# Optimization experiments

Measured on AMD Instinct MI355X. Metric: run time of the kernel, lower is better.

## Reference

```python
import jax, jax.numpy as jnp
import numpy as np


def setup_inputs() -> dict:
    key = jax.random.key(0)
    ks = jax.random.split(key, 8)
    B, L, D, N, K = 4, 4096, 1024, 64, 4
    return {
        "x": jax.random.normal(ks[0], (B, L, D), dtype=jnp.float32),
        "conv_w": jax.random.normal(ks[1], (K, 1, D), dtype=jnp.float32) * 0.1,
        "conv_b": jnp.zeros((D,), dtype=jnp.float32),
        "Wp": jax.random.normal(ks[2], (D, 2 * N), dtype=jnp.float32) * (1.0 / np.sqrt(D)),
        "bp": jnp.zeros((2 * N,), dtype=jnp.float32),
        "Ws": jax.random.normal(ks[3], (D, N), dtype=jnp.float32) * (1.0 / np.sqrt(D)),
        "bs": jnp.zeros((N,), dtype=jnp.float32),
        "A_log": jax.random.normal(ks[4], (N,), dtype=jnp.float32) * 0.02,
        "dt_log": jax.random.normal(ks[5], (N,), dtype=jnp.float32) * 0.02,
        "Wo": jax.random.normal(ks[6], (N, D), dtype=jnp.float32) * (1.0 / np.sqrt(N)),
        "bo": jnp.zeros((D,), dtype=jnp.float32),
    }


def reference(x, conv_w, conv_b, Wp, bp, Ws, bs, A_log, dt_log, Wo, bo):
    B, L, D = x.shape
    K = conv_w.shape[0]
    N = Ws.shape[1]

    # causal depthwise conv: left-pad by K-1, sum K shifted slices (K is tiny)
    x_pad = jnp.pad(x, ((0, 0), (K - 1, 0), (0, 0)))
    conv = conv_b + sum(x_pad[:, k:k + L, :] * conv_w[k, 0] for k in range(K))

    proj = conv @ Wp + bp                     # [B, L, 2N]
    B_t = jax.nn.softplus(proj[..., :N])      # [B, L, N]
    C_t = jnp.tanh(proj[..., N:])             # [B, L, N]
    u = x @ Ws + bs                           # [B, L, N]

    A = -jax.nn.softplus(A_log)               # [N]
    dt = jax.nn.softplus(dt_log)              # [N]
    decay = 1.0 + dt * A                      # [N]

    def step(state, inputs):
        u_t, b_t, c_t = inputs                # each [B, N]
        state = decay * state + dt * b_t * u_t
        return state, c_t * state

    init = jnp.zeros((B, N), dtype=x.dtype)
    xs = tuple(jnp.swapaxes(a, 0, 1) for a in (u, B_t, C_t))  # time-major
    _, ys = jax.lax.scan(step, init, xs, unroll=4)            # [L, B, N]
    y = jnp.swapaxes(ys, 0, 1)                                # [B, L, N]
    return y @ Wo + bo                                        # [B, L, D]
```

## Files before the change

### kernel.cpp

```cpp
#include <hip/hip_runtime.h>

#define B_ 4
#define L_ 4096
#define D_ 1024
#define N_ 64

typedef _Float16 f16;
typedef __attribute__((ext_vector_type(8))) _Float16 half8;
typedef __attribute__((ext_vector_type(4))) float f32x4;

__device__ __forceinline__ float softplus_f(float x) {
    return fmaxf(x, 0.0f) + log1pf(__expf(-fabsf(x)));
}

__device__ __forceinline__ float tanh_f(float x) {
    float xc = fminf(fmaxf(x, -15.0f), 15.0f);
    float e = __expf(2.0f * xc);
    return (e - 1.0f) / (e + 1.0f);
}

__global__ __launch_bounds__(256) void k_prepw(
    const float* __restrict__ Wp, const float* __restrict__ Ws,
    const float* __restrict__ Wo, f16* __restrict__ WT, f16* __restrict__ WoT)
{
    int gid = blockIdx.x * 256 + threadIdx.x;
    if (gid < 24576) {
        int r = gid >> 7, kg = gid & 127;
        const float* src; int ncol, c;
        if (r < 128) { src = Wp; ncol = 128; c = r; }
        else         { src = Ws; ncol = 64;  c = r - 128; }
        f16 h[8];
        #pragma unroll
        for (int j = 0; j < 8; j++)
            h[j] = (f16)src[(size_t)(kg * 8 + j) * ncol + c];
        *(uint4*)&WT[(size_t)r * 1024 + kg * 8] = *(uint4*)h;
    } else {
        int g2 = gid - 24576;
        int d = g2 >> 3, ng = g2 & 7;
        f16 h[8];
        #pragma unroll
        for (int j = 0; j < 8; j++)
            h[j] = (f16)Wo[(size_t)(ng * 8 + j) * D_ + d];
        *(uint4*)&WoT[(size_t)d * 64 + ng * 8] = *(uint4*)h;
    }
}

__global__ __launch_bounds__(256) void k_frontend(
    const float* __restrict__ x, const float* __restrict__ conv_w,
    const float* __restrict__ conv_b, const f16* __restrict__ WT,
    const float* __restrict__ bp, const float* __restrict__ bs,
    const float* __restrict__ dt_log,
    f16* __restrict__ zT, f16* __restrict__ cT)
{
    __shared__ __align__(16) char smem[25664];
    f16*   xh  = (f16*)smem;
    f16*   ch  = (f16*)(smem + 2880);
    float* cwS = (float*)(smem + 5184);
    float* sE  = (float*)smem;

    const int tid = threadIdx.x;
    const int w = tid >> 6, lane = tid & 63;
    const int r = lane & 15, q = lane >> 4;
    const int T0 = blockIdx.x * 16;
    const int bb = T0 >> 12;
    const int l0 = T0 & (L_ - 1);
    const int cw0 = w * 48;

    f32x4 acc[3] = {};
    float4 rA, rB;

    #pragma unroll
    for (int i = 0; i < 5; i++) {
        int idx = tid + 256 * i;
        float4 v = (idx < 1024) ? ((const float4*)conv_w)[idx]
                                : ((const float4*)conv_b)[idx - 1024];
        ((float4*)cwS)[idx] = v;
    }

    #define LDX(c0)                                                          \
        {                                                                    \
            {                                                                \
                int row = tid >> 4, g = tid & 15;                            \
                int l = l0 + row - 4;                                        \
                float4 v = make_float4(0.f, 0.f, 0.f, 0.f);                  \
                if (l >= 0)                                                  \
                    v = *(const float4*)&x[((size_t)(bb * L_ + l)) * D_      \
                                           + (c0) + g * 4];                  \
                rA = v;                                                      \
            }                                                                \
            if (tid < 64) {                                                  \
                int row = 16 + (tid >> 4), g = tid & 15;                     \
                int l = l0 + row - 4;               \
                rB = *(const float4*)&x[((size_t)(bb * L_ + l)) * D_         \
                                        + (c0) + g * 4];                     \
            }                                                                \
        }

    LDX(0);
    for (int c = 0; c < 16; c++) {
        __syncthreads();
        {
            int row = tid >> 4, g = tid & 15;
            f16 h[4] = {(f16)rA.x, (f16)rA.y, (f16)rA.z, (f16)rA.w};
            *(uint2*)&xh[row * 72 + g * 4] = *(uint2*)h;
            if (tid < 64) {
                int row2 = 16 + (tid >> 4);
                f16 h2[4] = {(f16)rB.x, (f16)rB.y, (f16)rB.z, (f16)rB.w};
                *(uint2*)&xh[row2 * 72 + g * 4] = *(uint2*)h2;
            }
        }
        __syncthreads();
        if (c < 15) LDX((c + 1) * 64);

        const int k0 = c * 64;

        half8 af[2][3];
        #pragma unroll
        for (int ks = 0; ks < 2; ks++)
            #pragma unroll
            for (int mf = 0; mf < 3; mf++)
                af[ks][mf] = *(const half8*)&WT[
                    (size_t)(cw0 + mf * 16 + r) * 1024 + k0 + ks * 32 + q * 8];

        {
            const int row = tid >> 4;
            const int d4 = (tid & 15) * 4;
            const int dg = k0 + d4;
            f32x4 w0 = *(const f32x4*)&cwS[dg];
            f32x4 w1 = *(const f32x4*)&cwS[1024 + dg];
            f32x4 w2 = *(const f32x4*)&cwS[2048 + dg];
            f32x4 w3 = *(const f32x4*)&cwS[3072 + dg];
            f32x4 cb = *(const f32x4*)&cwS[4096 + dg];
            f16 x0[4], x1[4], x2[4], x3[4], ho[4];
            *(uint2*)x0 = *(const uint2*)&xh[(row + 1) * 72 + d4];
            *(uint2*)x1 = *(const uint2*)&xh[(row + 2) * 72 + d4];
            *(uint2*)x2 = *(const uint2*)&xh[(row + 3) * 72 + d4];
            *(uint2*)x3 = *(const uint2*)&xh[(row + 4) * 72 + d4];
            #pragma unroll
            for (int j = 0; j < 4; j++) {
                float s = cb[j];
                s = fmaf(w0[j], (float)x0[j], s);
                s = fmaf(w1[j], (float)x1[j], s);
                s = fmaf(w2[j], (float)x2[j], s);
                s = fmaf(w3[j], (float)x3[j], s);
                ho[j] = (f16)s;
            }
            *(uint2*)&ch[row * 72 + d4] = *(uint2*)ho;
        }
        __syncthreads();

        const bool needC = (cw0 < 128);
        const bool needR = (cw0 + 32 >= 128);
        #pragma unroll
        for (int ks = 0; ks < 2; ks++) {
            const int kl = ks * 32 + q * 8;
            half8 bc = {}, br = {};
            if (needC) bc = *(const half8*)&ch[r * 72 + kl];
            if (needR) br = *(const half8*)&xh[(r + 4) * 72 + kl];
            #pragma unroll
            for (int mf = 0; mf < 3; mf++) {
                const bool useConv = (cw0 + mf * 16) < 128;
                acc[mf] = __builtin_amdgcn_mfma_f32_16x16x32_f16(
                    af[ks][mf], useConv ? bc : br, acc[mf], 0, 0, 0);
            }
        }
    }

    float* sB = sE;
    float* sC = sE + 16 * 68;
    float* sU = sE + 2 * 16 * 68;
    __syncthreads();
    #pragma unroll
    for (int mf = 0; mf < 3; mf++) {
        const int cb4 = cw0 + mf * 16 + q * 4;
        const int seg = cb4 >> 6;
        const int cl = cb4 & 63;
        const float4 bb4 = (seg == 2) ? *(const float4*)&bs[cl]
                                      : *(const float4*)&bp[cb4];
        float* dst = (seg == 0) ? sB : (seg == 1 ? sC : sU);
        const int t = r;
        float v0 = acc[mf][0] + bb4.x;
        float v1 = acc[mf][1] + bb4.y;
        float v2 = acc[mf][2] + bb4.z;
        float v3 = acc[mf][3] + bb4.w;
        if (seg == 0) {
            v0 = softplus_f(v0); v1 = softplus_f(v1);
            v2 = softplus_f(v2); v3 = softplus_f(v3);
        } else if (seg == 1) {
            v0 = tanh_f(v0); v1 = tanh_f(v1);
            v2 = tanh_f(v2); v3 = tanh_f(v3);
        }
        float4 vv = {v0, v1, v2, v3};
        *(float4*)&dst[t * 68 + cl] = vv;
    }
    __syncthreads();

    {
        const int n = tid >> 2, tg = tid & 3;
        const float dtv = softplus_f(dt_log[n]);
        f16 hz[4], hc[4];
        #pragma unroll
        for (int j = 0; j < 4; j++) {
            const int t = tg * 4 + j;
            hz[j] = (f16)(dtv * sB[t * 68 + n] * sU[t * 68 + n]);
            hc[j] = (f16)sC[t * 68 + n];
        }
        size_t o = ((size_t)(bb * N_ + n)) * L_ + l0 + tg * 4;
        *(uint2*)&zT[o] = *(uint2*)hz;
        *(uint2*)&cT[o] = *(uint2*)hc;
    }
    #undef LDX
}

__global__ __launch_bounds__(64) void k_scan(
    const f16* __restrict__ zT, const f16* __restrict__ cT,
    const float* __restrict__ A_log, const float* __restrict__ dt_log,
    f16* __restrict__ yH)
{
    __shared__ float zs[L_];
    __shared__ float cs[L_];
    const int bn = blockIdx.x;
    const int n = bn & (N_ - 1);
    const int lane = threadIdx.x;
    const f16* zp = zT + (size_t)bn * L_;
    const f16* cp = cT + (size_t)bn * L_;

    for (int it = 0; it < 8; it++) {
        int i = lane * 8 + it * 512;
        uint4 rz = *(const uint4*)(zp + i);
        uint4 rc = *(const uint4*)(cp + i);
        const f16* hz = (const f16*)&rz;
        const f16* hc = (const f16*)&rc;
        #pragma unroll
        for (int k = 0; k < 8; k++) {
            zs[i + k] = (float)hz[k];
            cs[i + k] = (float)hc[k];
        }
    }
    __syncthreads();

    float dtv = softplus_f(dt_log[n]);
    float Av = -softplus_f(A_log[n]);
    float dec = fmaf(dtv, Av, 1.0f);

    float s = 0.0f;
    const int base = lane * 64;
    #pragma unroll
    for (int j = 0; j < 64; j++) s = fmaf(dec, s, zs[base + j]);

    float d2 = dec * dec, d4 = d2 * d2, d8 = d4 * d4;
    float d16 = d8 * d8, d32 = d16 * d16, d64 = d32 * d32;

    float Ag = d64, Bg = s;
    #pragma unroll
    for (int off = 1; off < 64; off <<= 1) {
        float Ap = __shfl_up(Ag, off);
        float Bp = __shfl_up(Bg, off);
        if (lane >= off) { Bg = fmaf(Ag, Bp, Bg); Ag *= Ap; }
    }
    float carry = __shfl_up(Bg, 1);
    if (lane == 0) carry = 0.0f;

    float st = carry;
    #pragma unroll
    for (int j = 0; j < 64; j++) {
        st = fmaf(dec, st, zs[base + j]);
        zs[base + j] = cs[base + j] * st;
    }
    __syncthreads();
    f16* yp = yH + (size_t)bn * L_;
    for (int i = lane * 8; i < L_; i += 512) {
        f16 h[8];
        #pragma unroll
        for (int k = 0; k < 8; k++) h[k] = (f16)zs[i + k];
        *(uint4*)&yp[i] = *(uint4*)h;
    }
}

__global__ __launch_bounds__(256) void k_out(
    const f16* __restrict__ yH, const f16* __restrict__ WoT,
    const float* __restrict__ bo, float* __restrict__ out)
{
    __shared__ __align__(16) f16 ys[64 * 72];
    const int tid = threadIdx.x;
    const int w = tid >> 6, lane = tid & 63;
    const int r = lane & 15, q = lane >> 4;
    const int T0 = blockIdx.x * 64;
    const int bb = T0 >> 12, l0 = T0 & (L_ - 1);
    const int dw = blockIdx.y * 128 + w * 32;

    {
        const int n = tid & 63, tg = tid >> 6;
        #pragma unroll
        for (int h2 = 0; h2 < 2; h2++) {
            uint4 v = *(const uint4*)&yH[((size_t)(bb * N_ + n)) * L_ + l0 + tg * 16 + h2 * 8];
            const f16* hh = (const f16*)&v;
            #pragma unroll
            for (int j = 0; j < 8; j++)
                ys[(tg * 16 + h2 * 8 + j) * 72 + n] = hh[j];
        }
    }
    __syncthreads();

    f32x4 acc[2][4] = {};
    #pragma unroll
    for (int ks = 0; ks < 2; ks++) {
        const int kk = ks * 32 + q * 8;
        half8 af[2];
        #pragma unroll
        for (int mf = 0; mf < 2; mf++)
            af[mf] = *(const half8*)&WoT[(size_t)(dw + mf * 16 + r) * 64 + kk];
        #pragma unroll
        for (int nf = 0; nf < 4; nf++) {
            half8 bf = *(const half8*)&ys[(nf * 16 + r) * 72 + kk];
            #pragma unroll
            for (int mf = 0; mf < 2; mf++)
                acc[mf][nf] = __builtin_amdgcn_mfma_f32_16x16x32_f16(
                    af[mf], bf, acc[mf][nf], 0, 0, 0);
        }
    }

    #pragma unroll
    for (int mf = 0; mf < 2; mf++) {
        const int d = dw + mf * 16 + q * 4;
        const float4 bb4 = *(const float4*)&bo[d];
        #pragma unroll
        for (int nf = 0; nf < 4; nf++) {
            const int t = T0 + nf * 16 + r;
            float4 o = {acc[mf][nf][0] + bb4.x, acc[mf][nf][1] + bb4.y,
                        acc[mf][nf][2] + bb4.z, acc[mf][nf][3] + bb4.w};
            *(float4*)&out[(size_t)t * D_ + d] = o;
        }
    }
}

extern "C" void kernel_launch(void* const* d_in, const int* in_sizes, int n_in,
                              void* d_out, int out_size, void* d_ws, size_t ws_size,
                              hipStream_t stream) {
    const float* x      = (const float*)d_in[0];
    const float* conv_w = (const float*)d_in[1];
    const float* conv_b = (const float*)d_in[2];
    const float* Wp     = (const float*)d_in[3];
    const float* bp     = (const float*)d_in[4];
    const float* Ws     = (const float*)d_in[5];
    const float* bs     = (const float*)d_in[6];
    const float* A_log  = (const float*)d_in[7];
    const float* dt_log = (const float*)d_in[8];
    const float* Wo     = (const float*)d_in[9];
    const float* bo     = (const float*)d_in[10];
    float* out = (float*)d_out;

    char* wsp = (char*)d_ws;
    f16* WT  = (f16*)wsp;
    f16* WoT = (f16*)(wsp + 393216);
    f16* zT  = (f16*)(wsp + 524288);
    f16* cT  = (f16*)(wsp + 2621440);
    f16* yH  = (f16*)(wsp + 4718592);

    k_prepw<<<dim3(128), dim3(256), 0, stream>>>(Wp, Ws, Wo, WT, WoT);
    k_frontend<<<dim3(B_ * L_ / 16), dim3(256), 0, stream>>>(
        x, conv_w, conv_b, WT, bp, bs, dt_log, zT, cT);
    k_scan<<<dim3(B_ * N_), dim3(64), 0, stream>>>(zT, cT, A_log, dt_log, yH);
    k_out<<<dim3(B_ * L_ / 64, D_ / 128), dim3(256), 0, stream>>>(yH, WoT, bo, out);
}
```

Measured before the change: 198.1 us.

## Stage whole x tile in LDS for frontend and widen scan to four waves

The frontend now loads the full 20x1024 x tile into LDS at once (fp16, padded stride), computes the causal conv for all 16 rows in one pass using a sliding register window, and then runs a single uninterrupted MFMA loop over K. This drops the per-chunk double-buffered load/sync structure. LDS use grows to about 75KB per block, which cuts occupancy. The scan kernel moves from 64 to 256 threads with padded shared indexing and a two-level (wave, then cross-wave) scan, shortening each thread's serial chain from 64 to 16 steps.

```diff
diff --git a/kernel.cpp b/kernel.cpp
--- a/kernel.cpp
+++ b/kernel.cpp
@@ -45,6 +45,7 @@
     }
 }
 
+#define XS 1040
 __global__ __launch_bounds__(256) void k_frontend(
     const float* __restrict__ x, const float* __restrict__ conv_w,
     const float* __restrict__ conv_b, const f16* __restrict__ WT,
@@ -52,11 +53,10 @@
     const float* __restrict__ dt_log,
     f16* __restrict__ zT, f16* __restrict__ cT)
 {
-    __shared__ __align__(16) char smem[25664];
-    f16*   xh  = (f16*)smem;
-    f16*   ch  = (f16*)(smem + 2880);
-    float* cwS = (float*)(smem + 5184);
-    float* sE  = (float*)smem;
+    __shared__ __align__(16) char smem[74880];
+    f16*   xh = (f16*)smem;
+    f16*   ch = (f16*)(smem + 41600);
+    float* sE = (float*)smem;
 
     const int tid = threadIdx.x;
     const int w = tid >> 6, lane = tid & 63;
@@ -66,104 +66,75 @@
     const int l0 = T0 & (L_ - 1);
     const int cw0 = w * 48;
 
-    f32x4 acc[3] = {};
-    float4 rA, rB;
-
-    #pragma unroll
-    for (int i = 0; i < 5; i++) {
-        int idx = tid + 256 * i;
-        float4 v = (idx < 1024) ? ((const float4*)conv_w)[idx]
-                                : ((const float4*)conv_b)[idx - 1024];
-        ((float4*)cwS)[idx] = v;
-    }
-
-    #define LDX(c0)                                                          \
-        {                                                                    \
-            {                                                                \
-                int row = tid >> 4, g = tid & 15;                            \
-                int l = l0 + row - 4;                                        \
-                float4 v = make_float4(0.f, 0.f, 0.f, 0.f);                  \
-                if (l >= 0)                                                  \
-                    v = *(const float4*)&x[((size_t)(bb * L_ + l)) * D_      \
-                                           + (c0) + g * 4];                  \
-                rA = v;                                                      \
-            }                                                                \
-            if (tid < 64) {                                                  \
-                int row = 16 + (tid >> 4), g = tid & 15;                     \
-                int l = l0 + row - 4;               \
-                rB = *(const float4*)&x[((size_t)(bb * L_ + l)) * D_         \
-                                        + (c0) + g * 4];                     \
-            }                                                                \
-        }
-
-    LDX(0);
-    for (int c = 0; c < 16; c++) {
-        __syncthreads();
-        {
-            int row = tid >> 4, g = tid & 15;
-            f16 h[4] = {(f16)rA.x, (f16)rA.y, (f16)rA.z, (f16)rA.w};
-            *(uint2*)&xh[row * 72 + g * 4] = *(uint2*)h;
-            if (tid < 64) {
-                int row2 = 16 + (tid >> 4);
-                f16 h2[4] = {(f16)rB.x, (f16)rB.y, (f16)rB.z, (f16)rB.w};
-                *(uint2*)&xh[row2 * 72 + g * 4] = *(uint2*)h2;
-            }
-        }
-        __syncthreads();
-        if (c < 15) LDX((c + 1) * 64);
-
-        const int k0 = c * 64;
-
-        half8 af[2][3];
-        #pragma unroll
-        for (int ks = 0; ks < 2; ks++)
-            #pragma unroll
-            for (int mf = 0; mf < 3; mf++)
-                af[ks][mf] = *(const half8*)&WT[
-                    (size_t)(cw0 + mf * 16 + r) * 1024 + k0 + ks * 32 + q * 8];
-
-        {
-            const int row = tid >> 4;
-            const int d4 = (tid & 15) * 4;
-            const int dg = k0 + d4;
-            f32x4 w0 = *(const f32x4*)&cwS[dg];
-            f32x4 w1 = *(const f32x4*)&cwS[1024 + dg];
-            f32x4 w2 = *(const f32x4*)&cwS[2048 + dg];
-            f32x4 w3 = *(const f32x4*)&cwS[3072 + dg];
-            f32x4 cb = *(const f32x4*)&cwS[4096 + dg];
-            f16 x0[4], x1[4], x2[4], x3[4], ho[4];
-            *(uint2*)x0 = *(const uint2*)&xh[(row + 1) * 72 + d4];
-            *(uint2*)x1 = *(const uint2*)&xh[(row + 2) * 72 + d4];
-            *(uint2*)x2 = *(const uint2*)&xh[(row + 3) * 72 + d4];
-            *(uint2*)x3 = *(const uint2*)&xh[(row + 4) * 72 + d4];
+    #pragma unroll
+    for (int s = 0; s < 20; s++) {
+        int idx = tid + 256 * s;
+        int row = idx >> 8, g = idx & 255;
+        int l = l0 + row - 4;
+        float4 v = make_float4(0.f, 0.f, 0.f, 0.f);
+        if (l >= 0)
+            v = *(const float4*)&x[((size_t)(bb * L_ + l)) * D_ + g * 4];
+        f16 h[4] = {(f16)v.x, (f16)v.y, (f16)v.z, (f16)v.w};
+        *(uint2*)&xh[row * XS + g * 4] = *(uint2*)h;
+    }
+    __syncthreads();
+
+    {
+        const int d0 = tid * 4;
+        const float4 w0 = *(const float4*)&conv_w[0 * D_ + d0];
+        const float4 w1 = *(const float4*)&conv_w[1 * D_ + d0];
+        const float4 w2 = *(const float4*)&conv_w[2 * D_ + d0];
+        const float4 w3 = *(const float4*)&conv_w[3 * D_ + d0];
+        const float4 cb = *(const float4*)&conv_b[d0];
+        const float cwv[4][4] = {{w0.x,w0.y,w0.z,w0.w},{w1.x,w1.y,w1.z,w1.w},
+                                 {w2.x,w2.y,w2.z,w2.w},{w3.x,w3.y,w3.z,w3.w}};
+        const float cbv[4] = {cb.x, cb.y, cb.z, cb.w};
+        uint2 win[4];
+        win[0] = *(const uint2*)&xh[1 * XS + d0];
+        win[1] = *(const uint2*)&xh[2 * XS + d0];
+        win[2] = *(const uint2*)&xh[3 * XS + d0];
+        #pragma unroll
+        for (int t = 0; t < 16; t++) {
+            win[3] = *(const uint2*)&xh[(t + 4) * XS + d0];
+            const f16* x0 = (const f16*)&win[0];
+            const f16* x1 = (const f16*)&win[1];
+            const f16* x2 = (const f16*)&win[2];
+            const f16* x3 = (const f16*)&win[3];
+            f16 ho[4];
             #pragma unroll
             for (int j = 0; j < 4; j++) {
-                float s = cb[j];
-                s = fmaf(w0[j], (float)x0[j], s);
-                s = fmaf(w1[j], (float)x1[j], s);
-                s = fmaf(w2[j], (float)x2[j], s);
-                s = fmaf(w3[j], (float)x3[j], s);
+                float s = cbv[j];
+                s = fmaf(cwv[0][j], (float)x0[j], s);
+                s = fmaf(cwv[1][j], (float)x1[j], s);
+                s = fmaf(cwv[2][j], (float)x2[j], s);
+                s = fmaf(cwv[3][j], (float)x3[j], s);
                 ho[j] = (f16)s;
             }
-            *(uint2*)&ch[row * 72 + d4] = *(uint2*)ho;
-        }
-        __syncthreads();
-
-        const bool needC = (cw0 < 128);
-        const bool needR = (cw0 + 32 >= 128);
-        #pragma unroll
-        for (int ks = 0; ks < 2; ks++) {
-            const int kl = ks * 32 + q * 8;
-            half8 bc = {}, br = {};
-            if (needC) bc = *(const half8*)&ch[r * 72 + kl];
-            if (needR) br = *(const half8*)&xh[(r + 4) * 72 + kl];
-            #pragma unroll
-            for (int mf = 0; mf < 3; mf++) {
-                const bool useConv = (cw0 + mf * 16) < 128;
-                acc[mf] = __builtin_amdgcn_mfma_f32_16x16x32_f16(
-                    af[ks][mf], useConv ? bc : br, acc[mf], 0, 0, 0);
-            }
-        }
+            *(uint2*)&ch[t * XS + d0] = *(uint2*)ho;
+            win[0] = win[1]; win[1] = win[2]; win[2] = win[3];
+        }
+    }
+    __syncthreads();
+
+    f32x4 acc[3] = {};
+    const bool needC = (cw0 < 128);
+    const bool needR = (cw0 + 32 >= 128);
+    const bool uc0 = (cw0      < 128);
+    const bool uc1 = (cw0 + 16 < 128);
+    const bool uc2 = (cw0 + 32 < 128);
+    const int klq = q * 8;
+    #pragma unroll 4
+    for (int j = 0; j < 32; j++) {
+        const int kk = j * 32 + klq;
+        half8 a0 = *(const half8*)&WT[(size_t)(cw0 +      r) * 1024 + kk];
+        half8 a1 = *(const half8*)&WT[(size_t)(cw0 + 16 + r) * 1024 + kk];
+        half8 a2 = *(const half8*)&WT[(size_t)(cw0 + 32 + r) * 1024 + kk];
+        half8 bc = {}, br = {};
+        if (needC) bc = *(const half8*)&ch[r * XS + kk];
+        if (needR) br = *(const half8*)&xh[(r + 4) * XS + kk];
+        acc[0] = __builtin_amdgcn_mfma_f32_16x16x32_f16(a0, uc0 ? bc : br, acc[0], 0, 0, 0);
+        acc[1] = __builtin_amdgcn_mfma_f32_16x16x32_f16(a1, uc1 ? bc : br, acc[1], 0, 0, 0);
+        acc[2] = __builtin_amdgcn_mfma_f32_16x16x32_f16(a2, uc2 ? bc : br, acc[2], 0, 0, 0);
     }
 
     float* sB = sE;
@@ -178,7 +149,6 @@
         const float4 bb4 = (seg == 2) ? *(const float4*)&bs[cl]
                                       : *(const float4*)&bp[cb4];
         float* dst = (seg == 0) ? sB : (seg == 1 ? sC : sU);
-        const int t = r;
         float v0 = acc[mf][0] + bb4.x;
         float v1 = acc[mf][1] + bb4.y;
         float v2 = acc[mf][2] + bb4.z;
@@ -191,7 +161,7 @@
             v2 = tanh_f(v2); v3 = tanh_f(v3);
         }
         float4 vv = {v0, v1, v2, v3};
-        *(float4*)&dst[t * 68 + cl] = vv;
+        *(float4*)&dst[r * 68 + cl] = vv;
     }
     __syncthreads();
 
@@ -209,32 +179,36 @@
         *(uint2*)&zT[o] = *(uint2*)hz;
         *(uint2*)&cT[o] = *(uint2*)hc;
     }
-    #undef LDX
-}
-
-__global__ __launch_bounds__(64) void k_scan(
+}
+#undef XS
+
+#define ZI(i) ((i) + ((i) >> 4))
+__global__ __launch_bounds__(256) void k_scan(
     const f16* __restrict__ zT, const f16* __restrict__ cT,
     const float* __restrict__ A_log, const float* __restrict__ dt_log,
     f16* __restrict__ yH)
 {
-    __shared__ float zs[L_];
-    __shared__ float cs[L_];
+    __shared__ float zs[4352];
+    __shared__ float cs[4352];
+    __shared__ float sA[4], sB[4];
     const int bn = blockIdx.x;
     const int n = bn & (N_ - 1);
-    const int lane = threadIdx.x;
+    const int tid = threadIdx.x;
+    const int lane = tid & 63, w = tid >> 6;
     const f16* zp = zT + (size_t)bn * L_;
     const f16* cp = cT + (size_t)bn * L_;
 
-    for (int it = 0; it < 8; it++) {
-        int i = lane * 8 + it * 512;
+    #pragma unroll
+    for (int it = 0; it < 2; it++) {
+        int i = tid * 8 + it * 2048;
         uint4 rz = *(const uint4*)(zp + i);
         uint4 rc = *(const uint4*)(cp + i);
         const f16* hz = (const f16*)&rz;
         const f16* hc = (const f16*)&rc;
         #pragma unroll
         for (int k = 0; k < 8; k++) {
-            zs[i + k] = (float)hz[k];
-            cs[i + k] = (float)hc[k];
+            zs[ZI(i + k)] = (float)hz[k];
+            cs[ZI(i + k)] = (float)hc[k];
         }
     }
     __syncthreads();
@@ -243,39 +217,49 @@
     float Av = -softplus_f(A_log[n]);
     float dec = fmaf(dtv, Av, 1.0f);
 
+    const int base = tid * 17;
     float s = 0.0f;
-    const int base = lane * 64;
-    #pragma unroll
-    for (int j = 0; j < 64; j++) s = fmaf(dec, s, zs[base + j]);
-
-    float d2 = dec * dec, d4 = d2 * d2, d8 = d4 * d4;
-    float d16 = d8 * d8, d32 = d16 * d16, d64 = d32 * d32;
-
-    float Ag = d64, Bg = s;
+    #pragma unroll
+    for (int j = 0; j < 16; j++) s = fmaf(dec, s, zs[base + j]);
+
+    float d2 = dec * dec, d4 = d2 * d2, d8 = d4 * d4, d16 = d8 * d8;
+
+    float Ag = d16, Bg = s;
     #pragma unroll
     for (int off = 1; off < 64; off <<= 1) {
         float Ap = __shfl_up(Ag, off);
         float Bp = __shfl_up(Bg, off);
         if (lane >= off) { Bg = fmaf(Ag, Bp, Bg); Ag *= Ap; }
     }
-    float carry = __shfl_up(Bg, 1);
-    if (lane == 0) carry = 0.0f;
+    if (lane == 63) { sA[w] = Ag; sB[w] = Bg; }
+    __syncthreads();
+
+    float Bc = 0.0f;
+    for (int i = 0; i < w; i++) Bc = fmaf(sA[i], Bc, sB[i]);
+    float Ae = __shfl_up(Ag, 1);
+    float Be = __shfl_up(Bg, 1);
+    if (lane == 0) { Ae = 1.0f; Be = 0.0f; }
+    float carry = fmaf(Ae, Bc, Be);
 
     float st = carry;
     #pragma unroll
-    for (int j = 0; j < 64; j++) {
+    for (int j = 0; j < 16; j++) {
         st = fmaf(dec, st, zs[base + j]);
         zs[base + j] = cs[base + j] * st;
     }
     __syncthreads();
+
     f16* yp = yH + (size_t)bn * L_;
-    for (int i = lane * 8; i < L_; i += 512) {
+    #pragma unroll
+    for (int it = 0; it < 2; it++) {
+        int i = tid * 8 + it * 2048;
         f16 h[8];
         #pragma unroll
-        for (int k = 0; k < 8; k++) h[k] = (f16)zs[i + k];
+        for (int k = 0; k < 8; k++) h[k] = (f16)zs[ZI(i + k)];
         *(uint4*)&yp[i] = *(uint4*)h;
     }
 }
+#undef ZI
 
 __global__ __launch_bounds__(256) void k_out(
     const f16* __restrict__ yH, const f16* __restrict__ WoT,
@@ -360,6 +344,6 @@
     k_prepw<<<dim3(128), dim3(256), 0, stream>>>(Wp, Ws, Wo, WT, WoT);
     k_frontend<<<dim3(B_ * L_ / 16), dim3(256), 0, stream>>>(
         x, conv_w, conv_b, WT, bp, bs, dt_log, zT, cT);
-    k_scan<<<dim3(B_ * N_), dim3(64), 0, stream>>>(zT, cT, A_log, dt_log, yH);
+    k_scan<<<dim3(B_ * N_), dim3(256), 0, stream>>>(zT, cT, A_log, dt_log, yH);
     k_out<<<dim3(B_ * L_ / 64, D_ / 128), dim3(256), 0, stream>>>(yH, WoT, bo, out);
 }
```

Result: no change. 200.8 us (+1.4%).

## Parallelize scan across four waves with padded shared memory, reorder frontend loads

Applied to the files above, without the earlier changes.

The scan kernel now uses 256 threads per (batch, state) sequence instead of 64. Each thread handles 16 timesteps rather than 64, and a two-level prefix combine passes wave totals through shared memory. Shared-memory indices are padded every 16 elements to avoid bank conflicts on strided per-thread access. In the frontend, the weight-fragment loads and the next-chunk x prefetch move after the conv barrier, which changes register pressure and load overlap.

```diff
diff --git a/kernel.cpp b/kernel.cpp
--- a/kernel.cpp
+++ b/kernel.cpp
@@ -110,17 +110,8 @@
             }
         }
         __syncthreads();
-        if (c < 15) LDX((c + 1) * 64);
 
         const int k0 = c * 64;
-
-        half8 af[2][3];
-        #pragma unroll
-        for (int ks = 0; ks < 2; ks++)
-            #pragma unroll
-            for (int mf = 0; mf < 3; mf++)
-                af[ks][mf] = *(const half8*)&WT[
-                    (size_t)(cw0 + mf * 16 + r) * 1024 + k0 + ks * 32 + q * 8];
 
         {
             const int row = tid >> 4;
@@ -149,6 +140,16 @@
         }
         __syncthreads();
 
+        half8 af[2][3];
+        #pragma unroll
+        for (int ks = 0; ks < 2; ks++)
+            #pragma unroll
+            for (int mf = 0; mf < 3; mf++)
+                af[ks][mf] = *(const half8*)&WT[
+                    (size_t)(cw0 + mf * 16 + r) * 1024 + k0 + ks * 32 + q * 8];
+
+        if (c < 15) LDX((c + 1) * 64);
+
         const bool needC = (cw0 < 128);
         const bool needR = (cw0 + 32 >= 128);
         #pragma unroll
@@ -178,7 +179,6 @@
         const float4 bb4 = (seg == 2) ? *(const float4*)&bs[cl]
                                       : *(const float4*)&bp[cb4];
         float* dst = (seg == 0) ? sB : (seg == 1 ? sC : sU);
-        const int t = r;
         float v0 = acc[mf][0] + bb4.x;
         float v1 = acc[mf][1] + bb4.y;
         float v2 = acc[mf][2] + bb4.z;
@@ -191,7 +191,7 @@
             v2 = tanh_f(v2); v3 = tanh_f(v3);
         }
         float4 vv = {v0, v1, v2, v3};
-        *(float4*)&dst[t * 68 + cl] = vv;
+        *(float4*)&dst[r * 68 + cl] = vv;
     }
     __syncthreads();
 
@@ -212,29 +212,33 @@
     #undef LDX
 }
 
-__global__ __launch_bounds__(64) void k_scan(
+#define ZI(i) ((i) + ((i) >> 4))
+__global__ __launch_bounds__(256) void k_scan(
     const f16* __restrict__ zT, const f16* __restrict__ cT,
     const float* __restrict__ A_log, const float* __restrict__ dt_log,
     f16* __restrict__ yH)
 {
-    __shared__ float zs[L_];
-    __shared__ float cs[L_];
+    __shared__ float zs[4352];
+    __shared__ float cs[4352];
+    __shared__ float sA[4], sB[4];
     const int bn = blockIdx.x;
     const int n = bn & (N_ - 1);
-    const int lane = threadIdx.x;
+    const int tid = threadIdx.x;
+    const int lane = tid & 63, w = tid >> 6;
     const f16* zp = zT + (size_t)bn * L_;
     const f16* cp = cT + (size_t)bn * L_;
 
-    for (int it = 0; it < 8; it++) {
-        int i = lane * 8 + it * 512;
+    #pragma unroll
+    for (int it = 0; it < 2; it++) {
+        int i = tid * 8 + it * 2048;
         uint4 rz = *(const uint4*)(zp + i);
         uint4 rc = *(const uint4*)(cp + i);
         const f16* hz = (const f16*)&rz;
         const f16* hc = (const f16*)&rc;
         #pragma unroll
         for (int k = 0; k < 8; k++) {
-            zs[i + k] = (float)hz[k];
-            cs[i + k] = (float)hc[k];
+            zs[ZI(i + k)] = (float)hz[k];
+            cs[ZI(i + k)] = (float)hc[k];
         }
     }
     __syncthreads();
@@ -243,39 +247,49 @@
     float Av = -softplus_f(A_log[n]);
     float dec = fmaf(dtv, Av, 1.0f);
 
+    const int base = tid * 17;
     float s = 0.0f;
-    const int base = lane * 64;
-    #pragma unroll
-    for (int j = 0; j < 64; j++) s = fmaf(dec, s, zs[base + j]);
-
-    float d2 = dec * dec, d4 = d2 * d2, d8 = d4 * d4;
-    float d16 = d8 * d8, d32 = d16 * d16, d64 = d32 * d32;
-
-    float Ag = d64, Bg = s;
+    #pragma unroll
+    for (int j = 0; j < 16; j++) s = fmaf(dec, s, zs[base + j]);
+
+    float d2 = dec * dec, d4 = d2 * d2, d8 = d4 * d4, d16 = d8 * d8;
+
+    float Ag = d16, Bg = s;
     #pragma unroll
     for (int off = 1; off < 64; off <<= 1) {
         float Ap = __shfl_up(Ag, off);
         float Bp = __shfl_up(Bg, off);
         if (lane >= off) { Bg = fmaf(Ag, Bp, Bg); Ag *= Ap; }
     }
-    float carry = __shfl_up(Bg, 1);
-    if (lane == 0) carry = 0.0f;
+    if (lane == 63) { sA[w] = Ag; sB[w] = Bg; }
+    __syncthreads();
+
+    float Bc = 0.0f;
+    for (int i = 0; i < w; i++) Bc = fmaf(sA[i], Bc, sB[i]);
+    float Ae = __shfl_up(Ag, 1);
+    float Be = __shfl_up(Bg, 1);
+    if (lane == 0) { Ae = 1.0f; Be = 0.0f; }
+    float carry = fmaf(Ae, Bc, Be);
 
     float st = carry;
     #pragma unroll
-    for (int j = 0; j < 64; j++) {
+    for (int j = 0; j < 16; j++) {
         st = fmaf(dec, st, zs[base + j]);
         zs[base + j] = cs[base + j] * st;
     }
     __syncthreads();
+
     f16* yp = yH + (size_t)bn * L_;
-    for (int i = lane * 8; i < L_; i += 512) {
+    #pragma unroll
+    for (int it = 0; it < 2; it++) {
+        int i = tid * 8 + it * 2048;
         f16 h[8];
         #pragma unroll
-        for (int k = 0; k < 8; k++) h[k] = (f16)zs[i + k];
+        for (int k = 0; k < 8; k++) h[k] = (f16)zs[ZI(i + k)];
         *(uint4*)&yp[i] = *(uint4*)h;
     }
 }
+#undef ZI
 
 __global__ __launch_bounds__(256) void k_out(
     const f16* __restrict__ yH, const f16* __restrict__ WoT,
@@ -360,6 +374,6 @@
     k_prepw<<<dim3(128), dim3(256), 0, stream>>>(Wp, Ws, Wo, WT, WoT);
     k_frontend<<<dim3(B_ * L_ / 16), dim3(256), 0, stream>>>(
         x, conv_w, conv_b, WT, bp, bs, dt_log, zT, cT);
-    k_scan<<<dim3(B_ * N_), dim3(64), 0, stream>>>(zT, cT, A_log, dt_log, yH);
+    k_scan<<<dim3(B_ * N_), dim3(256), 0, stream>>>(zT, cT, A_log, dt_log, yH);
     k_out<<<dim3(B_ * L_ / 64, D_ / 128), dim3(256), 0, stream>>>(yH, WoT, bo, out);
 }
```

Measured after the change: 191.2 us. 1.04x faster.
